# Kernel optimization log

Measured on AMD Instinct MI355X. Metric: run time of the kernel, lower is better.

Reference implementation:

```python
import jax, jax.numpy as jnp
import numpy as np

CAPACITY = 0.5

def setup_inputs() -> dict:
    key = jax.random.key(0)
    kx, kw = jax.random.split(key)
    b, s, d = 4, 4096, 2048
    x = jax.random.normal(kx, (b, s, d), dtype=jnp.float32)
    # nn.Linear(d_model, 1, bias=False) weight: [1, d_model] -> store as [d_model]
    gate_w = jax.random.normal(kw, (d,), dtype=jnp.float32) * (1.0 / np.sqrt(d))
    return {"x": x, "gate_w": gate_w}

def reference(x, gate_w):
    b, s, _ = x.shape
    logits = jnp.einsum('bsd,d->bs', x, gate_w)            # [b, s]
    weights = jax.nn.sigmoid(logits.astype(jnp.float32)).astype(x.dtype)[..., None]  # [b, s, 1]
    num_selected = max(1, int(s * CAPACITY))
    if num_selected >= s:
        mask = jnp.ones_like(weights)
    else:
        _, top_idx = jax.lax.top_k(logits, num_selected)    # [b, k]
        mask2d = jnp.zeros((b, s), dtype=x.dtype).at[jnp.arange(b)[:, None], top_idx].set(1.0)
        mask = mask2d[..., None]                            # [b, s, 1]
    aux_loss = jnp.var(weights, ddof=1)                     # torch var is unbiased
    return mask, weights, aux_loss
```

## Files before the change

### kernel.cpp

```cpp
#include <hip/hip_runtime.h>
#include <hip/hip_bf16.h>

#define BATCH 4
#define SEQ   4096
#define DMODEL 2048
#define KSEL  2048

typedef float f32x4 __attribute__((ext_vector_type(4)));

__global__ __launch_bounds__(256) void logits_kernel(
    const float* __restrict__ x,
    const float* __restrict__ gate_w,
    float* __restrict__ logits,
    float* __restrict__ weights)
{
    const int wave = threadIdx.x >> 6;
    const int lane = threadIdx.x & 63;
    const int wid  = blockIdx.x * 4 + wave;
    const int row0 = wid * 2;

    const f32x4* wr = reinterpret_cast<const f32x4*>(gate_w);
    f32x4 wv[8];
#pragma unroll
    for (int t = 0; t < 8; ++t) wv[t] = wr[t * 64 + lane];

    double rsum[2];
#pragma unroll
    for (int r = 0; r < 2; ++r) {
        const f32x4* xr =
            reinterpret_cast<const f32x4*>(x + (size_t)(row0 + r) * DMODEL);
        f32x4 xv[8];
#pragma unroll
        for (int t = 0; t < 8; ++t) xv[t] = xr[t * 64 + lane];

        double a0 = 0.0, a1 = 0.0, a2 = 0.0, a3 = 0.0;
#pragma unroll
        for (int t = 0; t < 8; ++t) {
            a0 += (double)xv[t].x * (double)wv[t].x;
            a1 += (double)xv[t].y * (double)wv[t].y;
            a2 += (double)xv[t].z * (double)wv[t].z;
            a3 += (double)xv[t].w * (double)wv[t].w;
        }
        rsum[r] = (a0 + a1) + (a2 + a3);
    }

#pragma unroll
    for (int off = 32; off > 0; off >>= 1) {
        rsum[0] += __shfl_down(rsum[0], off, 64);
        rsum[1] += __shfl_down(rsum[1], off, 64);
    }

    if (lane == 0) {
#pragma unroll
        for (int r = 0; r < 2; ++r) {
            float l = (float)rsum[r];
            logits[row0 + r]  = l;
            weights[row0 + r] = 1.0f / (1.0f + expf(-l));
        }
    }
}

__global__ __launch_bounds__(512) void select_finalize_kernel(
    const float* __restrict__ logits,
    const float* __restrict__ weights,
    float* __restrict__ mask,
    float* __restrict__ aux)
{
    if (blockIdx.x == 512) {
        const int n = BATCH * SEQ;
        double s = 0.0, s2 = 0.0;
        for (int i = threadIdx.x; i < n; i += 512) {
            double w = (double)weights[i];
            s  += w;
            s2 += w * w;
        }
#pragma unroll
        for (int off = 32; off > 0; off >>= 1) {
            s  += __shfl_down(s,  off, 64);
            s2 += __shfl_down(s2, off, 64);
        }
        __shared__ double sh[16];
        const int wid  = threadIdx.x >> 6;
        const int lane = threadIdx.x & 63;
        if (lane == 0) { sh[wid] = s; sh[wid + 8] = s2; }
        __syncthreads();
        if (threadIdx.x == 0) {
            double S = 0.0, S2 = 0.0;
#pragma unroll
            for (int w = 0; w < 8; ++w) { S += sh[w]; S2 += sh[w + 8]; }
            double mean = S / n;
            double var  = (S2 - (double)n * mean * mean) / (double)(n - 1);
            *aux = (float)var;
        }
        return;
    }

    const int p    = blockIdx.x >> 1;
    const int h    = blockIdx.x & 1;
    const int b    = p >> 6;
    const int eblk = p & 63;

    __shared__ float L[SEQ];
    __shared__ int sh_gt[32][17];
    __shared__ int sh_eq[32][17];

    const float* row = logits + b * SEQ;
    for (int i = threadIdx.x; i < SEQ / 4; i += 512)
        reinterpret_cast<float4*>(L)[i] =
            reinterpret_cast<const float4*>(row)[i];
    __syncthreads();

    const int e     = threadIdx.x & 31;
    const int slice = threadIdx.x >> 5;
    const int i     = eblk * 64 + h * 32 + e;
    const float v   = L[i];

    int gt = 0, eq = 0;
    const int j0 = slice * (SEQ / 16);
#pragma unroll 4
    for (int j = j0; j < j0 + SEQ / 16; j += 4) {
        float4 q = *reinterpret_cast<const float4*>(&L[j]);
        gt += (q.x > v) + (q.y > v) + (q.z > v) + (q.w > v);
        eq += (q.x == v) + (q.y == v) + (q.z == v) + (q.w == v);
    }
    sh_gt[e][slice] = gt;
    sh_eq[e][slice] = eq;
    __syncthreads();

    if (slice == 0) {
        int GT = 0, EQ = 0;
#pragma unroll
        for (int s = 0; s < 16; ++s) { GT += sh_gt[e][s]; EQ += sh_eq[e][s]; }
        float m;
        if (GT >= KSEL) {
            m = 0.0f;
        } else if (EQ == 1) {
            m = 1.0f;
        } else {
            int lower = 0;
            for (int j = 0; j < i; ++j) lower += (L[j] == v);
            m = (GT + lower < KSEL) ? 1.0f : 0.0f;
        }
        mask[b * SEQ + i] = m;
    }
}

extern "C" void kernel_launch(void* const* d_in, const int* in_sizes, int n_in,
                              void* d_out, int out_size, void* d_ws, size_t ws_size,
                              hipStream_t stream) {
    const float* x      = (const float*)d_in[0];
    const float* gate_w = (const float*)d_in[1];

    float* out     = (float*)d_out;
    float* mask    = out;
    float* weights = out + BATCH * SEQ;
    float* aux     = out + 2 * BATCH * SEQ;

    float* logits = (float*)d_ws;

    logits_kernel<<<dim3(BATCH * SEQ / 8), dim3(256), 0, stream>>>(
        x, gate_w, logits, weights);

    select_finalize_kernel<<<dim3(513), dim3(512), 0, stream>>>(
        logits, weights, mask, aux);
}
```

Baseline: 42.44 us.

## Rank logits with wave ballot/popcount instead of per-thread shared-memory scans

The top-k selection kernel now keeps the row's logits in registers, eight per lane. For each of 64 candidate values it counts greater and equal entries with wave ballots and popcounts, replacing per-thread scalar comparisons over a shared-memory copy. Block count is halved because each block handles 64 candidates, and the shared-memory staging of the whole row is removed. In exchange the candidate value is broadcast from global or cache on every iteration, and the rare tie path now scans global memory.

```diff
diff --git a/kernel.cpp b/kernel.cpp
--- a/kernel.cpp
+++ b/kernel.cpp
@@ -66,7 +66,7 @@
     float* __restrict__ mask,
     float* __restrict__ aux)
 {
-    if (blockIdx.x == 512) {
+    if (blockIdx.x == 256) {
         const int n = BATCH * SEQ;
         double s = 0.0, s2 = 0.0;
         for (int i = threadIdx.x; i < n; i += 512) {
@@ -95,42 +95,44 @@
         return;
     }
 
-    const int p    = blockIdx.x >> 1;
-    const int h    = blockIdx.x & 1;
-    const int b    = p >> 6;
-    const int eblk = p & 63;
+    const int blk    = blockIdx.x;
+    const int b      = blk >> 6;
+    const int vchunk = blk & 63;
+    const float* row = logits + b * SEQ;
 
-    __shared__ float L[SEQ];
-    __shared__ int sh_gt[32][17];
-    __shared__ int sh_eq[32][17];
+    const int w = threadIdx.x >> 6;
+    const int l = threadIdx.x & 63;
 
-    const float* row = logits + b * SEQ;
-    for (int i = threadIdx.x; i < SEQ / 4; i += 512)
-        reinterpret_cast<float4*>(L)[i] =
-            reinterpret_cast<const float4*>(row)[i];
+    __shared__ unsigned int C[64][9];
+
+    float rv[8];
+#pragma unroll
+    for (int c = 0; c < 8; ++c) rv[c] = row[w * 512 + c * 64 + l];
+
+#pragma unroll 8
+    for (int k = 0; k < 64; ++k) {
+        const float vv = row[vchunk * 64 + k];
+        int gt = 0, eq = 0;
+#pragma unroll
+        for (int c = 0; c < 8; ++c) {
+            gt += __popcll(__ballot(rv[c] > vv));
+            eq += __popcll(__ballot(rv[c] == vv));
+        }
+        if (l == 0) C[k][w] = ((unsigned)gt << 16) | (unsigned)eq;
+    }
     __syncthreads();
 
-    const int e     = threadIdx.x & 31;
-    const int slice = threadIdx.x >> 5;
-    const int i     = eblk * 64 + h * 32 + e;
-    const float v   = L[i];
-
-    int gt = 0, eq = 0;
-    const int j0 = slice * (SEQ / 16);
-#pragma unroll 4
-    for (int j = j0; j < j0 + SEQ / 16; j += 4) {
-        float4 q = *reinterpret_cast<const float4*>(&L[j]);
-        gt += (q.x > v) + (q.y > v) + (q.z > v) + (q.w > v);
-        eq += (q.x == v) + (q.y == v) + (q.z == v) + (q.w == v);
-    }
-    sh_gt[e][slice] = gt;
-    sh_eq[e][slice] = eq;
-    __syncthreads();
-
-    if (slice == 0) {
-        int GT = 0, EQ = 0;
+    if (threadIdx.x < 64) {
+        const int k = threadIdx.x;
+        unsigned GT = 0, EQ = 0;
 #pragma unroll
-        for (int s = 0; s < 16; ++s) { GT += sh_gt[e][s]; EQ += sh_eq[e][s]; }
+        for (int ww = 0; ww < 8; ++ww) {
+            const unsigned p = C[k][ww];
+            GT += p >> 16;
+            EQ += p & 0xffffu;
+        }
+        const int i    = vchunk * 64 + k;
+        const float vv = row[i];
         float m;
         if (GT >= KSEL) {
             m = 0.0f;
@@ -138,7 +140,7 @@
             m = 1.0f;
         } else {
             int lower = 0;
-            for (int j = 0; j < i; ++j) lower += (L[j] == v);
+            for (int j = 0; j < i; ++j) lower += (row[j] == vv);
             m = (GT + lower < KSEL) ? 1.0f : 0.0f;
         }
         mask[b * SEQ + i] = m;
@@ -161,6 +163,6 @@
     logits_kernel<<<dim3(BATCH * SEQ / 8), dim3(256), 0, stream>>>(
         x, gate_w, logits, weights);
 
-    select_finalize_kernel<<<dim3(513), dim3(512), 0, stream>>>(
+    select_finalize_kernel<<<dim3(257), dim3(512), 0, stream>>>(
         logits, weights, mask, aux);
 }
```

Measured after the change: 41.26 us. 2.8% less time.
